# Kernel tuning notes

Hardware: AMD Instinct MI355X
Metric: run time of the kernel (lower is better)

## Reference

```python
import jax, jax.numpy as jnp
import numpy as np

B, NPER, K = 32, 256, 32
N, E = B * NPER, B * NPER * 32
H, NF, NG, L = 128, 128, 50, 6
CUTOFF = 10.0
LOG2 = 0.6931471805599453


def _ssp(x):
    # ShiftedSoftplus: softplus(x) - log(2)
    return jax.nn.softplus(x) - LOG2


def setup_inputs() -> dict:
    key = jax.random.key(0)
    ks = jax.random.split(key, 16)
    rng = np.random.default_rng(0)

    pos = jnp.asarray(rng.uniform(0.0, 5.0, size=(N, 3)).astype(np.float32))
    z = jnp.asarray(rng.integers(1, 100, size=(N,)).astype(np.int32))
    batch = jnp.asarray((np.arange(N) // NPER).astype(np.int32))
    # K neighbors per atom, within the same graph, no self-loops; dst sorted
    dst = np.repeat(np.arange(N), K)
    off = rng.integers(1, NPER, size=N * K)
    src = (dst % NPER + off) % NPER + (dst // NPER) * NPER
    edge_index = jnp.asarray(np.stack([src, dst]).astype(np.int32))
    domain_ids = jnp.asarray(rng.integers(0, 5, size=(B,)).astype(np.int32))

    def dense(k, i, o):
        return jax.random.normal(k, (i, o), jnp.float32) / np.sqrt(i)

    def stackw(k, i, o):
        return jax.random.normal(k, (L, i, o), jnp.float32) / np.sqrt(i)

    return {
        'pos': pos, 'z': z, 'batch': batch, 'edge_index': edge_index,
        'domain_ids': domain_ids,
        'embedding': jax.random.normal(ks[0], (100, H), jnp.float32),
        'mlp_w1': stackw(ks[1], NG, NF), 'mlp_b1': jnp.zeros((L, NF), jnp.float32),
        'mlp_w2': stackw(ks[2], NF, NF), 'mlp_b2': jnp.zeros((L, NF), jnp.float32),
        'cf_lin1_w': stackw(ks[3], H, NF),
        'cf_lin2_w': stackw(ks[4], NF, H), 'cf_lin2_b': jnp.zeros((L, H), jnp.float32),
        'int_lin_w': stackw(ks[5], H, H), 'int_lin_b': jnp.zeros((L, H), jnp.float32),
        'out_w1': dense(ks[6], H, H // 2), 'out_b1': jnp.zeros((H // 2,), jnp.float32),
        'out_w2': dense(ks[7], H // 2, 1), 'out_b2': jnp.zeros((1,), jnp.float32),
        'dom_emb': jax.random.normal(ks[8], (5, 64), jnp.float32),
        'film_w1': dense(ks[9], 64, 128), 'film_b1': jnp.zeros((128,), jnp.float32),
        'film_w2': dense(ks[10], 128, 128), 'film_b2': jnp.zeros((128,), jnp.float32),
        'gamma_w': dense(ks[11], 128, H), 'gamma_b': jnp.zeros((H,), jnp.float32),
        'beta_w': dense(ks[12], 128, H), 'beta_b': jnp.zeros((H,), jnp.float32),
    }


def reference(pos, z, batch, edge_index, domain_ids, embedding,
              mlp_w1, mlp_b1, mlp_w2, mlp_b2, cf_lin1_w, cf_lin2_w, cf_lin2_b,
              int_lin_w, int_lin_b, out_w1, out_b1, out_w2, out_b2,
              dom_emb, film_w1, film_b1, film_w2, film_b2,
              gamma_w, gamma_b, beta_w, beta_b):
    n_atoms = pos.shape[0]
    n_graphs = domain_ids.shape[0]
    src, dst = edge_index[0], edge_index[1]

    # edge distances, gaussian smearing, cosine cutoff (computed once)
    d = jnp.sqrt(jnp.sum((pos[src] - pos[dst]) ** 2, axis=-1))          # [E]
    offsets = jnp.linspace(0.0, CUTOFF, NG).astype(pos.dtype)
    coeff = -0.5 / (CUTOFF / (NG - 1)) ** 2
    edge_attr = jnp.exp(coeff * (d[:, None] - offsets) ** 2)            # [E,NG]
    C = 0.5 * (jnp.cos(d * (np.pi / CUTOFF)) + 1.0)                     # [E]

    h = embedding[z]                                                    # [N,H]
    for l in range(L):
        # filter network on gaussian basis, modulated by cosine cutoff
        W = (_ssp(edge_attr @ mlp_w1[l] + mlp_b1[l]) @ mlp_w2[l] + mlp_b2[l]) * C[:, None]  # [E,NF]
        x = h @ cf_lin1_w[l]                                            # [N,NF]
        msg = x[src] * W                                                # [E,NF]
        agg = jax.ops.segment_sum(msg, dst, num_segments=n_atoms)       # [N,NF]
        x = agg @ cf_lin2_w[l] + cf_lin2_b[l]                           # [N,H]
        h = h + _ssp(x) @ int_lin_w[l] + int_lin_b[l]                   # residual

    atom_e = _ssp(h @ out_w1 + out_b1) @ out_w2 + out_b2                # [N,1]
    e_graph = jax.ops.segment_sum(atom_e, batch, num_segments=n_graphs) # [B,1]

    # FiLM domain bias (features are zeros, so gamma path contributes 0 - faithful)
    de = dom_emb[domain_ids]                                            # [B,64]
    film = jax.nn.relu(de @ film_w1 + film_b1) @ film_w2 + film_b2      # [B,128]
    gamma = film @ gamma_w + gamma_b                                    # [B,H]
    beta = film @ beta_w + beta_b                                       # [B,H]
    dummy = jnp.zeros((n_graphs, H), pos.dtype)
    bias = jnp.sum(gamma * dummy + beta, axis=-1)                       # [B]

    # faithful broadcast [B,1]+[B] -> [B,B], then sum(dim=1) as in original
    energy = jnp.sum(e_graph + bias[None, :], axis=1)                   # [B]

    forces = jnp.zeros((n_atoms, 3), energy.dtype)
    stress = jnp.zeros((n_graphs, 3, 3), energy.dtype)
    features = jnp.zeros((n_atoms, H), energy.dtype)
    return energy, forces, stress, features
```

## Files before the change

kernel.cpp:

```cpp
#include <hip/hip_runtime.h>
#include <math.h>

using uint = unsigned int;
typedef _Float16 h2    __attribute__((ext_vector_type(2)));
typedef _Float16 f16x8 __attribute__((ext_vector_type(8)));
typedef float    f32x4 __attribute__((ext_vector_type(4)));

#define N_ATOMS 8192
#define NEDGE   262144
#define KNBR    32
#define NGAUSS  50
#define NLAYER  6
#define NB      32
#define GTAB    1024
#define DMAX    8.6603f
#define FCUT    10.0f
#define MB      1048576

#define NSETUP  512

#define LSTRIDE 76
#define S_WT    0
#define S_AS    9728

#define WA_OFF  0
#define WB_OFF  8192
#define AS_OFF  16384
#define TS_OFF  17408
#define LAY_N   18432

#define T_W1    0
#define T_W2    4096
#define T_RBF   12288
#define T_HID   13312
#define TAB_SMEM 15360

#define OW1P_OFF 147456
#define PACK_END 151552
#define X_STR    524288

__device__ __forceinline__ float ssp(float x) {
    return fmaxf(x, 0.0f) + log1pf(expf(-fabsf(x))) - 0.69314718055994531f;
}
__device__ __forceinline__ uint pack2(float a, float b) {
    union { h2 h; uint u; } x;
    h2 v; v.x = (_Float16)a; v.y = (_Float16)b; x.h = v; return x.u;
}
__device__ __forceinline__ h2 u2h(uint u) {
    union { uint u; h2 h; } x; x.u = u; return x.h;
}
__device__ __forceinline__ uint h2u(h2 h) {
    union { h2 h; uint u; } x; x.h = h; return x.u;
}
__device__ __forceinline__ float fdot2f(h2 a, h2 b, float c) {
#if __has_builtin(__builtin_amdgcn_fdot2)
    return __builtin_amdgcn_fdot2(a, b, c, false);
#else
    return fmaf((float)a.y, (float)b.y, fmaf((float)a.x, (float)b.x, c));
#endif
}

__device__ __forceinline__ int swz(int row, int quad) {
    return row * 64 + ((quad ^ (row & 15)) << 2);
}
__device__ __forceinline__ int swzc(int row, int c) {
    return row * 64 + (((c >> 2) ^ (row & 15)) << 2) + (c & 3);
}

__device__ __forceinline__ void stage_sw(uint* dst, const uint* __restrict__ src,
                                         int n16, int tid) {
    for (int i = tid; i < n16; i += 256) {
        uint4 v = ((const uint4*)src)[i];
        *(uint4*)&dst[swz(i >> 4, i & 15)] = v;
    }
}

template<int NCT>
__device__ __forceinline__ void run_gemm_sw(const uint* smA, const uint* smW,
                                            int lane, int nb, f32x4* acc) {
    int m = lane & 15, q = lane >> 4;
    #pragma unroll
    for (int ks = 0; ks < 4; ++ks) {
        int cq = q + ks * 4;
        f16x8 a = *(const f16x8*)&smA[swz(m, cq)];
        #pragma unroll
        for (int ct = 0; ct < NCT; ++ct) {
            int n = nb + ct * 16 + m;
            f16x8 b = *(const f16x8*)&smW[swz(n, cq)];
            acc[ct] = __builtin_amdgcn_mfma_f32_16x16x32_f16(a, b, acc[ct], 0, 0, 0);
        }
    }
}

template<int NCT>
__device__ __forceinline__ void run_gemm(const uint* sm, int as_off, int lane,
                                         int nb, f32x4* acc) {
    int m = lane & 15, q = lane >> 4;
    #pragma unroll
    for (int ks = 0; ks < 4; ++ks) {
        f16x8 a = *(const f16x8*)&sm[as_off + m * LSTRIDE + q * 4 + ks * 16];
        #pragma unroll
        for (int ct = 0; ct < NCT; ++ct) {
            f16x8 b = *(const f16x8*)&sm[S_WT + (nb + ct * 16 + m) * LSTRIDE + q * 4 + ks * 16];
            acc[ct] = __builtin_amdgcn_mfma_f32_16x16x32_f16(a, b, acc[ct], 0, 0, 0);
        }
    }
}

struct SArgs {
    const float *pos; const int *z; const int *ei; const int *dom;
    const float *emb;
    const float *cf1; const float *cf2w; const float *intw; const float *ow1;
    const float *dome; const float *fw1; const float *fb1;
    const float *fw2; const float *fb2; const float *bw; const float *bb;
    uint2 *epack; float *h; uint *xA;
    float *gbias; uint *wpack; uint *bar;
    float *out; int out_size;
};

__global__ void __launch_bounds__(256) k_setup(SArgs a) {
    __shared__ __align__(16) uint sm[S_AS + 1216];
    const int tid = threadIdx.x, bid = blockIdx.x;
    const int gidx = bid * 256 + tid, gsz = NSETUP * 256;
    const int lane = tid & 63, w = tid >> 6;
    const int m = lane & 15, q = lane >> 4;
    const int rowbase = bid * 16;

    for (int i = gidx; i < a.out_size; i += gsz) a.out[i] = 0.0f;
    if (gidx < 256) a.bar[gidx] = 0u;

    for (int idx = gidx; idx < PACK_END; idx += gsz) {
        if (idx < OW1P_OFF) {
            int mat = idx >> 13, e = idx & 8191;
            int kp = e >> 7, cc = e & 127;
            const float* src = (mat < 6) ? (a.cf1 + mat * 16384)
                            : (mat < 12) ? (a.cf2w + (mat - 6) * 16384)
                                         : (a.intw + (mat - 12) * 16384);
            a.wpack[mat * 8192 + cc * 64 + kp] =
                pack2(src[2 * kp * 128 + cc], src[(2 * kp + 1) * 128 + cc]);
        } else {
            int e = idx - OW1P_OFF;
            int kp = e >> 6, cc = e & 63;
            a.wpack[OW1P_OFF + cc * 64 + kp] =
                pack2(a.ow1[2 * kp * 64 + cc], a.ow1[(2 * kp + 1) * 64 + cc]);
        }
    }

    const float invdelta = (float)(GTAB - 1) / DMAX;
    #pragma unroll
    for (int t = 0; t < 2; ++t) {
        int e = rowbase * KNBR + t * 256 + tid;
        int s = a.ei[e], d = a.ei[NEDGE + e];
        float dx = a.pos[3*s] - a.pos[3*d];
        float dy = a.pos[3*s+1] - a.pos[3*d+1];
        float dz = a.pos[3*s+2] - a.pos[3*d+2];
        float dist = sqrtf(dx*dx + dy*dy + dz*dz);
        float u = dist * invdelta;
        int i0 = (int)u; i0 = (i0 < GTAB - 2) ? i0 : (GTAB - 2);
        float t2 = u - (float)i0;
        uint tb = pack2(t2, 0.0f) & 0xffffu;
        uint2 ep; ep.x = (uint)s; ep.y = (tb << 16) | (uint)i0;
        a.epack[e] = ep;
    }

    for (int i = tid; i < 1024; i += 256) {
        int r = i >> 6, f2 = i & 63;
        int zz = a.z[rowbase + r];
        float2 v = *(const float2*)&a.emb[zz * 128 + f2 * 2];
        *(float2*)&a.h[(rowbase + r) * 128 + f2 * 2] = v;
        sm[S_AS + r * LSTRIDE + f2] = pack2(v.x, v.y);
    }
    for (int i = tid; i < 2048; i += 256) {
        int m4 = i >> 7, cc = i & 127;
        float v[8];
        #pragma unroll
        for (int j = 0; j < 8; ++j) v[j] = a.cf1[(8 * m4 + j) * 128 + cc];
        uint4 pk; pk.x = pack2(v[0], v[1]); pk.y = pack2(v[2], v[3]);
        pk.z = pack2(v[4], v[5]); pk.w = pack2(v[6], v[7]);
        *(uint4*)&sm[cc * LSTRIDE + m4 * 4] = pk;
    }
    __syncthreads();
    {
        f32x4 acc[2] = {{0,0,0,0},{0,0,0,0}};
        run_gemm<2>(sm, S_AS, lane, w * 32, acc);
        #pragma unroll
        for (int ct = 0; ct < 2; ++ct) {
            int n = w * 32 + ct * 16 + m;
            #pragma unroll
            for (int i = 0; i < 4; ++i) {
                float v = acc[ct][i];
                float u = __shfl_xor(v, 1, 64);
                if (!(lane & 1))
                    a.xA[(rowbase + q * 4 + i) * 64 + (n >> 1)] = pack2(v, u);
            }
        }
    }
    __syncthreads();
    if (bid >= 32 && bid < 64) {
        int g = bid - 32;
        float* fs = (float*)sm;
        if (tid < 64) fs[tid] = a.dome[a.dom[g] * 64 + tid];
        __syncthreads();
        if (tid < 128) {
            float acc = a.fb1[tid];
            for (int i = 0; i < 64; ++i) acc = fmaf(fs[i], a.fw1[i*128 + tid], acc);
            fs[64 + tid] = fmaxf(acc, 0.0f);
        }
        __syncthreads();
        if (tid < 128) {
            float acc = a.fb2[tid];
            for (int i = 0; i < 128; ++i) acc = fmaf(fs[64+i], a.fw2[i*128 + tid], acc);
            fs[192 + tid] = acc;
        }
        __syncthreads();
        if (tid < 128) {
            float acc = a.bb[tid];
            for (int i = 0; i < 128; ++i) acc = fmaf(fs[192+i], a.bw[i*128 + tid], acc);
            #pragma unroll
            for (int off = 32; off > 0; off >>= 1) acc += __shfl_down(acc, off, 64);
            if ((tid & 63) == 0) fs[320 + (tid >> 6)] = acc;
        }
        __syncthreads();
        if (tid == 0) a.gbias[g] = fs[320] + fs[321];
    }
}

__global__ void __launch_bounds__(256) k_table(
    const float* __restrict__ mw1, const float* __restrict__ mb1,
    const float* __restrict__ mw2, const float* __restrict__ mb2,
    uint* __restrict__ tab2) {
    __shared__ __align__(16) uint sm[TAB_SMEM];
    const int tid = threadIdx.x;
    const int l = blockIdx.x >> 5;
    const int base = (blockIdx.x & 31) * 32;
    for (int i = tid; i < 4096; i += 256) {
        int kp = i >> 7, cc = i & 127, g0 = 2 * kp;
        float va = (g0 < NGAUSS)     ? mw1[l*NGAUSS*128 + g0*128 + cc]     : 0.f;
        float vb = (g0 + 1 < NGAUSS) ? mw1[l*NGAUSS*128 + (g0+1)*128 + cc] : 0.f;
        sm[T_W1 + i] = pack2(va, vb);
    }
    for (int i = tid; i < 8192; i += 256) {
        int kp = i >> 7, cc = i & 127;
        sm[T_W2 + i] = pack2(mw2[l*16384 + 2*kp*128 + cc],
                             mw2[l*16384 + (2*kp+1)*128 + cc]);
    }
    const float delta = DMAX / (float)(GTAB - 1);
    const float gstep = FCUT / (float)(NGAUSS - 1);
    const float coeff = -0.5f / (gstep * gstep);
    for (int i = tid; i < 1024; i += 256) {
        int r = i >> 5, kp = i & 31;
        float dv = (float)(base + r) * delta;
        int g0 = 2 * kp;
        float v0 = 0.f, v1 = 0.f;
        if (g0 < NGAUSS)     { float t = dv - (float)g0 * gstep;     v0 = expf(coeff*t*t); }
        if (g0 + 1 < NGAUSS) { float t = dv - (float)(g0+1) * gstep; v1 = expf(coeff*t*t); }
        sm[T_RBF + i] = pack2(v0, v1);
    }
    __syncthreads();
    int tx = tid & 31, ty = tid >> 5, c0 = tx * 4, tr0 = ty * 4;
    float acc[4][4];
    #pragma unroll
    for (int i = 0; i < 4; ++i) { acc[i][0]=0.f; acc[i][1]=0.f; acc[i][2]=0.f; acc[i][3]=0.f; }
    #pragma unroll
    for (int oct = 0; oct < 8; ++oct) {
        int kp0 = oct * 4;
        uint4 w_[4];
        #pragma unroll
        for (int p = 0; p < 4; ++p) w_[p] = *(const uint4*)&sm[T_W1 + (kp0+p)*128 + c0];
        #pragma unroll
        for (int i = 0; i < 4; ++i) {
            uint4 av = *(const uint4*)&sm[T_RBF + (tr0+i)*32 + kp0];
            uint aa[4] = {av.x, av.y, av.z, av.w};
            #pragma unroll
            for (int p = 0; p < 4; ++p) {
                h2 ap = u2h(aa[p]);
                acc[i][0] = fdot2f(ap, u2h(w_[p].x), acc[i][0]);
                acc[i][1] = fdot2f(ap, u2h(w_[p].y), acc[i][1]);
                acc[i][2] = fdot2f(ap, u2h(w_[p].z), acc[i][2]);
                acc[i][3] = fdot2f(ap, u2h(w_[p].w), acc[i][3]);
            }
        }
    }
    float4 b1v = *(const float4*)&mb1[l*128 + c0];
    #pragma unroll
    for (int i = 0; i < 4; ++i) {
        uint2 o;
        o.x = pack2(ssp(acc[i][0] + b1v.x), ssp(acc[i][1] + b1v.y));
        o.y = pack2(ssp(acc[i][2] + b1v.z), ssp(acc[i][3] + b1v.w));
        *(uint2*)&sm[T_HID + (tr0+i)*64 + (c0 >> 1)] = o;
    }
    __syncthreads();
    float acc2[4][4];
    #pragma unroll
    for (int i = 0; i < 4; ++i) { acc2[i][0]=0.f; acc2[i][1]=0.f; acc2[i][2]=0.f; acc2[i][3]=0.f; }
    #pragma unroll 4
    for (int oct = 0; oct < 16; ++oct) {
        int kp0 = oct * 4;
        uint4 w_[4];
        #pragma unroll
        for (int p = 0; p < 4; ++p) w_[p] = *(const uint4*)&sm[T_W2 + (kp0+p)*128 + c0];
        #pragma unroll
        for (int i = 0; i < 4; ++i) {
            uint4 av = *(const uint4*)&sm[T_HID + (tr0+i)*64 + kp0];
            uint aa[4] = {av.x, av.y, av.z, av.w};
            #pragma unroll
            for (int p = 0; p < 4; ++p) {
                h2 ap = u2h(aa[p]);
                acc2[i][0] = fdot2f(ap, u2h(w_[p].x), acc2[i][0]);
                acc2[i][1] = fdot2f(ap, u2h(w_[p].y), acc2[i][1]);
                acc2[i][2] = fdot2f(ap, u2h(w_[p].z), acc2[i][2]);
                acc2[i][3] = fdot2f(ap, u2h(w_[p].w), acc2[i][3]);
            }
        }
    }
    float4 b2v = *(const float4*)&mb2[l*128 + c0];
    #pragma unroll
    for (int i = 0; i < 4; ++i) {
        int row = base + tr0 + i;
        float dv = (float)row * delta;
        float Cd = 0.5f * (cosf(dv * 0.3141592653589793f) + 1.0f);
        uint2 o;
        o.x = pack2((acc2[i][0] + b2v.x)*Cd, (acc2[i][1] + b2v.y)*Cd);
        o.y = pack2((acc2[i][2] + b2v.z)*Cd, (acc2[i][3] + b2v.w)*Cd);
        *(uint2*)&tab2[(l*GTAB + row)*128 + tx*4] = o;
        if (row > 0)
            *(uint2*)&tab2[(l*GTAB + row - 1)*128 + tx*4 + 2] = o;
    }
}

struct LArgs {
    const float* h;
    const uint* x0;
    uint* xb;
    const uint* tab2;
    const uint2* epack;
    const uint* wpack;
    const float* cf2b;
    const float* intb;
    const float* ob1; const float* ow2; const float* ob2;
    const float* gbias;
    float* out;
    uint* bar;
};

__global__ void __launch_bounds__(256, 2) k_fused(LArgs a) {
    __shared__ __align__(16) uint sm[LAY_N];
    const int tid = threadIdx.x, bid = blockIdx.x;
    const int lane = tid & 63, w = tid >> 6;
    const int m = lane & 15, q = lane >> 4;
    const int xcd = bid & 7;
    const int j   = bid >> 3;
    const int g   = xcd * 4 + (j >> 4);
    const int sub = j & 15;
    const int rowbase = g * 256 + sub * 16;

    float hr[2][4];
    #pragma unroll
    for (int ct = 0; ct < 2; ++ct)
        #pragma unroll
        for (int i = 0; i < 4; ++i)
            hr[ct][i] = a.h[(rowbase + q * 4 + i) * 128 + w * 32 + ct * 16 + m];

    const uint* xr = a.x0;
    uint* xw = a.xb;

    #pragma unroll 1
    for (int l = 0; l < NLAYER; ++l) {
        const bool last = (l == NLAYER - 1);
        const uint* w2p  = a.wpack + (6 + l) * 8192;
        const uint* w3p  = a.wpack + (12 + l) * 8192;
        const uint* w1np = last ? (a.wpack + OW1P_OFF) : (a.wpack + (l + 1) * 8192);
        const uint* tabl = a.tab2 + l * (GTAB * 128);
        const float* b2 = a.cf2b + l * 128;
        const float* b3 = a.intb + l * 128;

        stage_sw(&sm[WA_OFF], w2p, 2048, tid);
        {
            const int side = lane >> 5, l5 = lane & 31;
            #pragma unroll
            for (int p = 0; p < 4; ++p) {
                int al = p * 4 + w;
                uint2 ep = a.epack[(rowbase + al) * KNBR + l5];
                h2 a0; a0.x = (_Float16)0; a0.y = (_Float16)0;
                h2 a1 = a0;
                #pragma unroll 4
                for (int k = 0; k < 16; ++k) {
                    int e = 2 * k + side;
                    uint s = __shfl(ep.x, e, 64);
                    uint y = __shfl(ep.y, e, 64);
                    int i0 = (int)(y & 0xffffu);
                    uint th = y >> 16;
                    h2 t2 = u2h(th | (th << 16));
                    uint4 tv = *(const uint4*)&tabl[i0 * 128 + l5 * 4];
                    uint2 xv = *(const uint2*)&xr[(int)s * 64 + l5 * 2];
                    h2 w0 = u2h(tv.x) + t2 * (u2h(tv.z) - u2h(tv.x));
                    h2 w1 = u2h(tv.y) + t2 * (u2h(tv.w) - u2h(tv.y));
                    a0 = a0 + u2h(xv.x) * w0;
                    a1 = a1 + u2h(xv.y) * w1;
                }
                uint u0 = h2u(a0), u1 = h2u(a1);
                uint p0 = __shfl_xor(u0, 32, 64), p1 = __shfl_xor(u1, 32, 64);
                if (side == 0) {
                    h2 r0 = u2h(u0) + u2h(p0), r1 = u2h(u1) + u2h(p1);
                    uint2 o; o.x = h2u(r0); o.y = h2u(r1);
                    *(uint2*)&sm[AS_OFF + swzc(al, l5 * 2)] = o;
                }
            }
        }
        __syncthreads();
        stage_sw(&sm[WB_OFF], w3p, 2048, tid);
        {
            f32x4 acc[2] = {{0,0,0,0},{0,0,0,0}};
            run_gemm_sw<2>(&sm[AS_OFF], &sm[WA_OFF], lane, w * 32, acc);
            #pragma unroll
            for (int ct = 0; ct < 2; ++ct) {
                int n = w * 32 + ct * 16 + m;
                float bv = b2[n];
                #pragma unroll
                for (int i = 0; i < 4; ++i) {
                    float v = ssp(acc[ct][i] + bv);
                    float u = __shfl_xor(v, 1, 64);
                    if (!(lane & 1))
                        sm[TS_OFF + swzc(q * 4 + i, n >> 1)] = pack2(v, u);
                }
            }
        }
        __syncthreads();
        stage_sw(&sm[WA_OFF], w1np, last ? 1024 : 2048, tid);
        {
            f32x4 acc[2] = {{0,0,0,0},{0,0,0,0}};
            run_gemm_sw<2>(&sm[TS_OFF], &sm[WB_OFF], lane, w * 32, acc);
            #pragma unroll
            for (int ct = 0; ct < 2; ++ct) {
                int n = w * 32 + ct * 16 + m;
                float bv = b3[n];
                #pragma unroll
                for (int i = 0; i < 4; ++i) {
                    float hv = hr[ct][i] + acc[ct][i] + bv;
                    hr[ct][i] = hv;
                    float u = __shfl_xor(hv, 1, 64);
                    if (!(lane & 1))
                        sm[AS_OFF + swzc(q * 4 + i, n >> 1)] = pack2(hv, u);
                }
            }
        }
        __syncthreads();
        if (!last) {
            f32x4 acc[2] = {{0,0,0,0},{0,0,0,0}};
            run_gemm_sw<2>(&sm[AS_OFF], &sm[WA_OFF], lane, w * 32, acc);
            #pragma unroll
            for (int ct = 0; ct < 2; ++ct) {
                int n = w * 32 + ct * 16 + m;
                #pragma unroll
                for (int i = 0; i < 4; ++i) {
                    float v = acc[ct][i];
                    float u = __shfl_xor(v, 1, 64);
                    if (!(lane & 1))
                        xw[(rowbase + q * 4 + i) * 64 + (n >> 1)] = pack2(v, u);
                }
            }
            __syncthreads();
            if (tid == 0) {
                uint* c = a.bar + l * NB + g;
                __hip_atomic_fetch_add(c, 1u, __ATOMIC_RELAXED,
                                       __HIP_MEMORY_SCOPE_SYSTEM);
                int it = 0;
                while (__hip_atomic_load(c, __ATOMIC_RELAXED,
                                         __HIP_MEMORY_SCOPE_SYSTEM) < 16u
                       && ++it < (1 << 18))
                    __builtin_amdgcn_s_sleep(2);
            }
            __syncthreads();
            xr = xw; xw += X_STR;
        } else {
            f32x4 acc[1] = {{0,0,0,0}};
            run_gemm_sw<1>(&sm[AS_OFF], &sm[WA_OFF], lane, w * 16, acc);
            int n = w * 16 + m;
            float b1v = a.ob1[n], w2v = a.ow2[n];
            float part = 0.f;
            #pragma unroll
            for (int i = 0; i < 4; ++i) part += ssp(acc[0][i] + b1v) * w2v;
            #pragma unroll
            for (int mm = 1; mm < 64; mm <<= 1) part += __shfl_xor(part, mm, 64);
            float* fs = (float*)&sm[TS_OFF];
            if (lane == 0) fs[w] = part;
            __syncthreads();
            if (tid == 0) {
                float bsum = fs[0] + fs[1] + fs[2] + fs[3] + 16.0f * a.ob2[0];
                float add = 32.0f * bsum;
                if (sub == 0) {
                    float sb = 0.f;
                    for (int jj = 0; jj < NB; ++jj) sb += a.gbias[jj];
                    add += sb;
                }
                atomicAdd(&a.out[g], add);
            }
        }
    }
}

extern "C" void kernel_launch(void* const* d_in, const int* in_sizes, int n_in,
                              void* d_out, int out_size, void* d_ws, size_t ws_size,
                              hipStream_t stream) {
    SArgs a;
    a.pos  = (const float*)d_in[0];
    a.z    = (const int*)d_in[1];
    a.ei   = (const int*)d_in[3];
    a.dom  = (const int*)d_in[4];
    a.emb  = (const float*)d_in[5];
    const float* mw1 = (const float*)d_in[6];
    const float* mb1 = (const float*)d_in[7];
    const float* mw2 = (const float*)d_in[8];
    const float* mb2 = (const float*)d_in[9];
    a.cf1  = (const float*)d_in[10];
    a.cf2w = (const float*)d_in[11];
    const float* cf2b = (const float*)d_in[12];
    a.intw = (const float*)d_in[13];
    const float* intb = (const float*)d_in[14];
    a.ow1  = (const float*)d_in[15];
    const float* ob1  = (const float*)d_in[16];
    const float* ow2  = (const float*)d_in[17];
    const float* ob2  = (const float*)d_in[18];
    a.dome = (const float*)d_in[19];
    a.fw1  = (const float*)d_in[20];
    a.fb1  = (const float*)d_in[21];
    a.fw2  = (const float*)d_in[22];
    a.fb2  = (const float*)d_in[23];
    a.bw   = (const float*)d_in[26];
    a.bb   = (const float*)d_in[27];

    char* ws = (char*)d_ws;
    a.epack   = (uint2*)(ws + 0);
    uint* tab2= (uint*)(ws + 2*MB);
    a.h       = (float*)(ws + 5*MB);
    a.xA      = (uint*)(ws + 9*MB);
    uint* xb  = (uint*)(ws + 11*MB);
    a.gbias   = (float*)(ws + 21*MB);
    a.bar     = (uint*)(ws + 21*MB + 4096);
    a.wpack   = (uint*)(ws + 21*MB + 8192);
    a.out = (float*)d_out;
    a.out_size = out_size;

    k_setup<<<NSETUP, 256, 0, stream>>>(a);
    k_table<<<192, 256, 0, stream>>>(mw1, mb1, mw2, mb2, tab2);

    LArgs la;
    la.h = a.h; la.x0 = a.xA; la.xb = xb;
    la.tab2 = tab2; la.epack = a.epack; la.wpack = a.wpack;
    la.cf2b = cf2b; la.intb = intb;
    la.ob1 = ob1; la.ow2 = ow2; la.ob2 = ob2;
    la.gbias = a.gbias; la.out = (float*)d_out; la.bar = a.bar;

    k_fused<<<dim3(512), dim3(256), 0, stream>>>(la);
}
```

Before: 272.6 us.

## Replace interpolated filter table with denser nearest-neighbor table and compact edge packing

Doubles the distance-filter lookup table resolution and switches from linear interpolation between two table rows to a nearest-entry lookup. This halves the table row width read per edge and drops the interpolation arithmetic. Edge records shrink from 8 to 4 bytes by packing the source index and table index into one word. The inter-block barrier atomics move from system to agent scope with a shorter sleep. The trade-off is a small accuracy loss from nearest-entry quantization and a larger table precompute, which now uses twice as many blocks.

```diff
diff --git a/kernel.cpp b/kernel.cpp
--- a/kernel.cpp
+++ b/kernel.cpp
@@ -12,7 +12,7 @@
 #define NGAUSS  50
 #define NLAYER  6
 #define NB      32
-#define GTAB    1024
+#define GTAB    2048
 #define DMAX    8.6603f
 #define FCUT    10.0f
 #define MB      1048576
@@ -113,7 +113,7 @@
     const float *cf1; const float *cf2w; const float *intw; const float *ow1;
     const float *dome; const float *fw1; const float *fb1;
     const float *fw2; const float *fb2; const float *bw; const float *bb;
-    uint2 *epack; float *h; uint *xA;
+    uint *epack; float *h; uint *xA;
     float *gbias; uint *wpack; uint *bar;
     float *out; int out_size;
 };
@@ -156,11 +156,8 @@
         float dz = a.pos[3*s+2] - a.pos[3*d+2];
         float dist = sqrtf(dx*dx + dy*dy + dz*dz);
         float u = dist * invdelta;
-        int i0 = (int)u; i0 = (i0 < GTAB - 2) ? i0 : (GTAB - 2);
-        float t2 = u - (float)i0;
-        uint tb = pack2(t2, 0.0f) & 0xffffu;
-        uint2 ep; ep.x = (uint)s; ep.y = (tb << 16) | (uint)i0;
-        a.epack[e] = ep;
+        int i0 = (int)(u + 0.5f); i0 = (i0 < GTAB - 1) ? i0 : (GTAB - 1);
+        a.epack[e] = (uint)s | ((uint)i0 << 16);
     }
 
     for (int i = tid; i < 1024; i += 256) {
@@ -228,11 +225,11 @@
 __global__ void __launch_bounds__(256) k_table(
     const float* __restrict__ mw1, const float* __restrict__ mb1,
     const float* __restrict__ mw2, const float* __restrict__ mb2,
-    uint* __restrict__ tab2) {
+    uint* __restrict__ tab) {
     __shared__ __align__(16) uint sm[TAB_SMEM];
     const int tid = threadIdx.x;
-    const int l = blockIdx.x >> 5;
-    const int base = (blockIdx.x & 31) * 32;
+    const int l = blockIdx.x >> 6;
+    const int base = (blockIdx.x & 63) * 32;
     for (int i = tid; i < 4096; i += 256) {
         int kp = i >> 7, cc = i & 127, g0 = 2 * kp;
         float va = (g0 < NGAUSS)     ? mw1[l*NGAUSS*128 + g0*128 + cc]     : 0.f;
@@ -322,9 +319,7 @@
         uint2 o;
         o.x = pack2((acc2[i][0] + b2v.x)*Cd, (acc2[i][1] + b2v.y)*Cd);
         o.y = pack2((acc2[i][2] + b2v.z)*Cd, (acc2[i][3] + b2v.w)*Cd);
-        *(uint2*)&tab2[(l*GTAB + row)*128 + tx*4] = o;
-        if (row > 0)
-            *(uint2*)&tab2[(l*GTAB + row - 1)*128 + tx*4 + 2] = o;
+        *(uint2*)&tab[(l*GTAB + row)*64 + tx*2] = o;
     }
 }
 
@@ -332,8 +327,8 @@
     const float* h;
     const uint* x0;
     uint* xb;
-    const uint* tab2;
-    const uint2* epack;
+    const uint* tab;
+    const uint* epack;
     const uint* wpack;
     const float* cf2b;
     const float* intb;
@@ -370,7 +365,7 @@
         const uint* w2p  = a.wpack + (6 + l) * 8192;
         const uint* w3p  = a.wpack + (12 + l) * 8192;
         const uint* w1np = last ? (a.wpack + OW1P_OFF) : (a.wpack + (l + 1) * 8192);
-        const uint* tabl = a.tab2 + l * (GTAB * 128);
+        const uint* tabl = a.tab + l * (GTAB * 64);
         const float* b2 = a.cf2b + l * 128;
         const float* b3 = a.intb + l * 128;
 
@@ -380,23 +375,16 @@
             #pragma unroll
             for (int p = 0; p < 4; ++p) {
                 int al = p * 4 + w;
-                uint2 ep = a.epack[(rowbase + al) * KNBR + l5];
+                uint ep = a.epack[(rowbase + al) * KNBR + l5];
                 h2 a0; a0.x = (_Float16)0; a0.y = (_Float16)0;
                 h2 a1 = a0;
                 #pragma unroll 4
                 for (int k = 0; k < 16; ++k) {
-                    int e = 2 * k + side;
-                    uint s = __shfl(ep.x, e, 64);
-                    uint y = __shfl(ep.y, e, 64);
-                    int i0 = (int)(y & 0xffffu);
-                    uint th = y >> 16;
-                    h2 t2 = u2h(th | (th << 16));
-                    uint4 tv = *(const uint4*)&tabl[i0 * 128 + l5 * 4];
-                    uint2 xv = *(const uint2*)&xr[(int)s * 64 + l5 * 2];
-                    h2 w0 = u2h(tv.x) + t2 * (u2h(tv.z) - u2h(tv.x));
-                    h2 w1 = u2h(tv.y) + t2 * (u2h(tv.w) - u2h(tv.y));
-                    a0 = a0 + u2h(xv.x) * w0;
-                    a1 = a1 + u2h(xv.y) * w1;
+                    uint v = __shfl(ep, 2 * k + side, 64);
+                    uint2 tv = *(const uint2*)&tabl[(v >> 16) * 64 + l5 * 2];
+                    uint2 xv = *(const uint2*)&xr[(v & 0xffffu) * 64 + l5 * 2];
+                    a0 = a0 + u2h(xv.x) * u2h(tv.x);
+                    a1 = a1 + u2h(xv.y) * u2h(tv.y);
                 }
                 uint u0 = h2u(a0), u1 = h2u(a1);
                 uint p0 = __shfl_xor(u0, 32, 64), p1 = __shfl_xor(u1, 32, 64);
@@ -463,12 +451,12 @@
             if (tid == 0) {
                 uint* c = a.bar + l * NB + g;
                 __hip_atomic_fetch_add(c, 1u, __ATOMIC_RELAXED,
-                                       __HIP_MEMORY_SCOPE_SYSTEM);
+                                       __HIP_MEMORY_SCOPE_AGENT);
                 int it = 0;
                 while (__hip_atomic_load(c, __ATOMIC_RELAXED,
-                                         __HIP_MEMORY_SCOPE_SYSTEM) < 16u
-                       && ++it < (1 << 18))
-                    __builtin_amdgcn_s_sleep(2);
+                                         __HIP_MEMORY_SCOPE_AGENT) < 16u
+                       && ++it < (1 << 19))
+                    __builtin_amdgcn_s_sleep(1);
             }
             __syncthreads();
             xr = xw; xw += X_STR;
@@ -530,8 +518,8 @@
     a.bb   = (const float*)d_in[27];
 
     char* ws = (char*)d_ws;
-    a.epack   = (uint2*)(ws + 0);
-    uint* tab2= (uint*)(ws + 2*MB);
+    a.epack   = (uint*)(ws + 0);
+    uint* tab = (uint*)(ws + 2*MB);
     a.h       = (float*)(ws + 5*MB);
     a.xA      = (uint*)(ws + 9*MB);
     uint* xb  = (uint*)(ws + 11*MB);
@@ -542,11 +530,11 @@
     a.out_size = out_size;
 
     k_setup<<<NSETUP, 256, 0, stream>>>(a);
-    k_table<<<192, 256, 0, stream>>>(mw1, mb1, mw2, mb2, tab2);
+    k_table<<<384, 256, 0, stream>>>(mw1, mb1, mw2, mb2, tab);
 
     LArgs la;
     la.h = a.h; la.x0 = a.xA; la.xb = xb;
-    la.tab2 = tab2; la.epack = a.epack; la.wpack = a.wpack;
+    la.tab = tab; la.epack = a.epack; la.wpack = a.wpack;
     la.cf2b = cf2b; la.intb = intb;
     la.ob1 = ob1; la.ow2 = ow2; la.ob2 = ob2;
     la.gbias = a.gbias; la.out = (float*)d_out; la.bar = a.bar;
```

Result: no change. 275.6 us (+1.1%).
